# Kernel optimization log

Measured on AMD Instinct MI355X. Metric: run time of the kernel, lower is better.

Reference implementation:

```python
import jax, jax.numpy as jnp
import numpy as np

B, S, DIM, HDIM = 8, 1024, 1024, 128
H = DIM // HDIM  # 8 heads
GN_EPS = 1e-3    # keras GroupNormalization default epsilon


def group_norm(y, gamma, beta, groups, eps=GN_EPS):
    # keras GroupNormalization on [B,S,C]: reshape to [B,S,groups,C//groups],
    # normalize over all axes except batch and group axis -> axes (1,3).
    b, s, c = y.shape
    g = y.reshape(b, s, groups, c // groups)
    mean = g.mean(axis=(1, 3), keepdims=True)
    var = g.var(axis=(1, 3), keepdims=True)
    g = (g - mean) * jax.lax.rsqrt(var + eps)
    return g.reshape(b, s, c) * gamma + beta


def setup_inputs() -> dict:
    key = jax.random.key(0)
    ks = jax.random.split(key, 7)
    x = jax.random.normal(ks[0], (B, S, DIM), dtype=jnp.float32)
    sc_h = 1.0 / np.sqrt(HDIM).astype(np.float32)
    sc_d = 1.0 / np.sqrt(DIM).astype(np.float32)
    Wq = jax.random.normal(ks[1], (H, HDIM, HDIM), dtype=jnp.float32) * sc_h
    Wk = jax.random.normal(ks[2], (H, HDIM, HDIM), dtype=jnp.float32) * sc_h
    Wv = jax.random.normal(ks[3], (H, HDIM, HDIM), dtype=jnp.float32) * sc_h
    Wg = jax.random.normal(ks[4], (DIM, DIM), dtype=jnp.float32) * sc_d
    Wo = jax.random.normal(ks[5], (DIM, DIM), dtype=jnp.float32) * sc_d
    gn_gamma = jnp.ones((DIM,), dtype=jnp.float32)
    gn_beta = jnp.zeros((DIM,), dtype=jnp.float32)
    return {"x": x, "Wq": Wq, "Wk": Wk, "Wv": Wv, "Wg": Wg, "Wo": Wo,
            "gn_gamma": gn_gamma, "gn_beta": gn_beta}


def reference(x, Wq, Wk, Wv, Wg, Wo, gn_gamma, gn_beta):
    b, s, c = x.shape
    h, hd = Wq.shape[0], Wq.shape[1]
    # gating branch: W = ReLU(x @ Wg)
    Wgate = jax.nn.relu(jnp.einsum('bsc,cd->bsd', x, Wg))
    # split channels into heads: [B,S,H,hd]
    xh = x.reshape(b, s, h, hd)
    Q = jnp.einsum('bshd,hde->bhse', xh, Wq)
    K = jnp.einsum('bshd,hde->bhse', xh, Wk)
    V = jnp.einsum('bshd,hde->bhse', xh, Wv)
    # per-head decay mask D[h,i,j] = gamma_h ** (i - j) (full, non-causal as in source)
    idx = jnp.arange(s, dtype=jnp.float32)
    gammas = 1.0 - 2.0 ** (-5.0 - jnp.arange(h, dtype=jnp.float32))  # [H]
    decay = gammas[:, None, None] ** (idx[None, :, None] - idx[None, None, :])  # [H,S,S]
    scores = jnp.einsum('bhsd,bhtd->bhst', Q, K) * decay[None]
    ret = jnp.einsum('bhst,bhtd->bhsd', scores, V)       # [B,H,S,hd]
    y = ret.transpose(0, 2, 1, 3).reshape(b, s, c)        # concat heads
    Y = group_norm(y, gn_gamma, gn_beta, groups=hd)       # groups = hdim (keras arg)
    return jnp.einsum('bsc,cd->bsd', Wgate * Y, Wo)
```

## Files before the change

### kernel.cpp

```cpp
#include <hip/hip_runtime.h>

#define BB 8
#define SS 1024
#define DD 1024
#define HH 8
#define HD 128
#define GN_EPS 1e-3f

typedef __attribute__((ext_vector_type(8))) short bf16x8;
typedef __attribute__((ext_vector_type(4))) float f32x4;

__device__ __forceinline__ short f2bf(float f) {
    unsigned u = __float_as_uint(f);
    return (short)((u + 0x7fffu + ((u >> 16) & 1u)) >> 16);
}
__device__ __forceinline__ float bf2f(short s) {
    return __uint_as_float(((unsigned)(unsigned short)s) << 16);
}

__device__ __forceinline__ void gload16(const void* g, void* l) {
    __builtin_amdgcn_global_load_lds((const __attribute__((address_space(1))) void*)g,
                                     (__attribute__((address_space(3))) void*)l, 16, 0, 0);
}

__device__ __forceinline__ void stage_tile(const short* __restrict__ G, size_t ld, int k0,
                                           short* lds, int wid, int lane) {
#pragma unroll
    for (int i = 0; i < 2; i++) {
        const int seg = wid * 2 + i;
        const int row = seg * 8 + (lane >> 3);
        const int chunk = (lane & 7) ^ (lane >> 3);
        gload16(G + (size_t)row * ld + k0 + chunk * 8, lds + seg * 512);
    }
}

__device__ __forceinline__ void gemm_tile_g(
    const short* __restrict__ A, size_t ldA,
    const short* __restrict__ B, size_t ldB,
    int K, short* As, short* Bs, f32x4 acc[4][2])
{
    const int tid = threadIdx.x, lane = tid & 63, wid = tid >> 6;
    const int wr = (wid >> 2) * 64, wc = (wid & 3) * 32;
    const int fr = lane & 15, fc = lane >> 4;
    const int rsw = fr & 7;
#pragma unroll
    for (int i = 0; i < 4; i++)
#pragma unroll
        for (int j = 0; j < 2; j++) acc[i][j] = (f32x4){0.f, 0.f, 0.f, 0.f};

    const int nt = K >> 6;
    stage_tile(A, ldA, 0, As, wid, lane);
    stage_tile(B, ldB, 0, Bs, wid, lane);
    if (nt > 1) {
        stage_tile(A, ldA, 64, As + 8192, wid, lane);
        stage_tile(B, ldB, 64, Bs + 8192, wid, lane);
    }
    for (int t = 0; t < nt; t++) {
        if (t + 1 < nt) asm volatile("s_waitcnt vmcnt(4)" ::: "memory");
        else            asm volatile("s_waitcnt vmcnt(0)" ::: "memory");
        __builtin_amdgcn_s_barrier();
        __builtin_amdgcn_sched_barrier(0);
        const int cur = t & 1;
        const short* as = As + (cur << 13);
        const short* bs = Bs + (cur << 13);
#pragma unroll
        for (int half = 0; half < 2; half++) {
            const int slot = ((half * 4 + fc) ^ rsw) << 3;
            bf16x8 af[4], bfv[2];
#pragma unroll
            for (int i = 0; i < 4; i++) af[i] = *(const bf16x8*)&as[(wr + i * 16 + fr) * 64 + slot];
#pragma unroll
            for (int j = 0; j < 2; j++) bfv[j] = *(const bf16x8*)&bs[(wc + j * 16 + fr) * 64 + slot];
#pragma unroll
            for (int i = 0; i < 4; i++)
#pragma unroll
                for (int j = 0; j < 2; j++)
                    acc[i][j] = __builtin_amdgcn_mfma_f32_16x16x32_bf16(af[i], bfv[j], acc[i][j], 0, 0, 0);
        }
        __builtin_amdgcn_sched_barrier(0);
        asm volatile("s_waitcnt lgkmcnt(0)" ::: "memory");
        __builtin_amdgcn_s_barrier();
        if (t + 2 < nt) {
            stage_tile(A, ldA, (t + 2) << 6, As + (cur << 13), wid, lane);
            stage_tile(B, ldB, (t + 2) << 6, Bs + (cur << 13), wid, lane);
        }
    }
}

__global__ __launch_bounds__(256) void prep(
    const float* __restrict__ x,
    const float* __restrict__ Wq, const float* __restrict__ Wk, const float* __restrict__ Wv,
    const float* __restrict__ Wg, const float* __restrict__ Wo,
    short* __restrict__ xb, short* __restrict__ WgT, short* __restrict__ WoT,
    short* __restrict__ Wt, float* __restrict__ sQ, float* __restrict__ sK,
    float* __restrict__ Sp)
{
    __shared__ float t[32][33];
    int bid = blockIdx.x;
    const int tid = threadIdx.x;
    if (bid < 4096) {
        const size_t i = ((size_t)bid * 256 + tid) * 8;
        float4 a = *(const float4*)&x[i];
        float4 b = *(const float4*)&x[i + 4];
        bf16x8 v;
        v[0] = f2bf(a.x); v[1] = f2bf(a.y); v[2] = f2bf(a.z); v[3] = f2bf(a.w);
        v[4] = f2bf(b.x); v[5] = f2bf(b.y); v[6] = f2bf(b.z); v[7] = f2bf(b.w);
        *(bf16x8*)&xb[i] = v;
        return;
    }
    bid -= 4096;
    if (bid < 2048) {
        const float* __restrict__ S = (bid < 1024) ? Wg : Wo;
        short* __restrict__ D = (bid < 1024) ? WgT : WoT;
        const int tb = bid & 1023;
        const int bx = (tb & 31) * 32, by = (tb >> 5) * 32;
        const int xx = tid & 31, y0 = tid >> 5;
#pragma unroll
        for (int r = 0; r < 32; r += 8) t[y0 + r][xx] = S[(size_t)(by + y0 + r) * 1024 + bx + xx];
        __syncthreads();
#pragma unroll
        for (int r = 0; r < 32; r += 8) D[(size_t)(bx + y0 + r) * 1024 + by + xx] = f2bf(t[xx][y0 + r]);
        return;
    }
    bid -= 2048;
    if (bid < 384) {
        const int ht = bid >> 4, tb = bid & 15;
        const int typ = ht >> 3, h = ht & 7;
        const float* __restrict__ W = (typ == 0 ? Wq : (typ == 1 ? Wk : Wv)) + (size_t)h * HD * HD;
        short* __restrict__ D = Wt + (size_t)ht * HD * HD;
        const int bx = (tb & 3) * 32, by = (tb >> 2) * 32;
        const int xx = tid & 31, y0 = tid >> 5;
#pragma unroll
        for (int r = 0; r < 32; r += 8) t[y0 + r][xx] = W[(by + y0 + r) * HD + bx + xx];
        __syncthreads();
#pragma unroll
        for (int r = 0; r < 32; r += 8) D[(bx + y0 + r) * HD + by + xx] = f2bf(t[xx][y0 + r]);
        return;
    }
    bid -= 384;
    if (bid < 32) {
        const int h = bid >> 2;
        const int s = (bid & 3) * 256 + tid;
        const double gamma = 1.0 - exp2((double)(-5 - h));
        const double lg = log2(gamma);
        sQ[h * SS + s] = (float)exp2(lg * (double)s);
        sK[h * SS + s] = (float)exp2(-lg * (double)s);
        return;
    }
    *(float4*)&Sp[tid * 8] = (float4){0.f, 0.f, 0.f, 0.f};
    *(float4*)&Sp[tid * 8 + 4] = (float4){0.f, 0.f, 0.f, 0.f};
}

__global__ __launch_bounds__(512) void g_qkvgate(
    const short* __restrict__ xb, const short* __restrict__ Wt, const short* __restrict__ WgT,
    const float* __restrict__ sQ, const float* __restrict__ sK,
    short* __restrict__ Qb, short* __restrict__ Ktb, short* __restrict__ Vtb,
    short* __restrict__ gateb)
{
    __shared__ short As[2 * 8192], Bs[2 * 8192];
    f32x4 acc[4][2];
    const int orig = blockIdx.x;
    const int cx = orig & 7, p = orig >> 3;
    const int tid = threadIdx.x, lane = tid & 63, wid = tid >> 6;
    const int wr = (wid >> 2) * 64, wc = (wid & 3) * 32;
    const int r0 = (lane >> 4) * 4, c = lane & 15;

    if (p < 64) {
        const int w2 = cx * 64 + p;
        const int m0 = (w2 >> 3) * 128, n0 = (w2 & 7) * 128;
        gemm_tile_g(xb + (size_t)m0 * DD, DD, WgT + (size_t)n0 * DD, DD, DD, As, Bs, acc);
#pragma unroll
        for (int i = 0; i < 4; i++)
#pragma unroll
            for (int j = 0; j < 2; j++)
#pragma unroll
                for (int r = 0; r < 4; r++)
                    gateb[(size_t)(m0 + wr + i * 16 + r0 + r) * DD + n0 + wc + j * 16 + c] =
                        f2bf(fmaxf(acc[i][j][r], 0.f));
        return;
    }
    const int w = cx * 192 + (p - 64);
    const int ht = w >> 6, mt = w & 63;
    const int m0 = mt * 128;
    const int typ = ht >> 3, h = ht & 7;
    gemm_tile_g(xb + (size_t)m0 * DD + h * HD, DD,
                Wt + (size_t)ht * HD * HD, HD, HD, As, Bs, acc);
    const int b = m0 >> 10, s0 = m0 & (SS - 1);
    const int bh = (b << 3) + h;
    if (typ == 0) {
#pragma unroll
        for (int i = 0; i < 4; i++)
#pragma unroll
            for (int j = 0; j < 2; j++)
#pragma unroll
                for (int r = 0; r < 4; r++) {
                    const int s = s0 + wr + i * 16 + r0 + r;
                    Qb[((size_t)bh * SS + s) * HD + wc + j * 16 + c] =
                        f2bf(acc[i][j][r] * sQ[h * SS + s]);
                }
    } else if (typ == 1) {
        short* __restrict__ Ob = Ktb + (size_t)bh * HD * SS;
#pragma unroll
        for (int i = 0; i < 4; i++)
#pragma unroll
            for (int j = 0; j < 2; j++) {
                const int tb = s0 + wr + i * 16 + r0;
                const int d = wc + j * 16 + c;
                short4 o;
                o.x = f2bf(acc[i][j][0] * sK[h * SS + tb + 0]);
                o.y = f2bf(acc[i][j][1] * sK[h * SS + tb + 1]);
                o.z = f2bf(acc[i][j][2] * sK[h * SS + tb + 2]);
                o.w = f2bf(acc[i][j][3] * sK[h * SS + tb + 3]);
                *(short4*)&Ob[(size_t)d * SS + tb] = o;
            }
    } else {
        short* __restrict__ Ob = Vtb + (size_t)bh * HD * SS;
#pragma unroll
        for (int i = 0; i < 4; i++)
#pragma unroll
            for (int j = 0; j < 2; j++) {
                const int tb = s0 + wr + i * 16 + r0;
                const int e = wc + j * 16 + c;
                short4 o;
                o.x = f2bf(acc[i][j][0]); o.y = f2bf(acc[i][j][1]);
                o.z = f2bf(acc[i][j][2]); o.w = f2bf(acc[i][j][3]);
                *(short4*)&Ob[(size_t)e * SS + tb] = o;
            }
    }
}

__global__ __launch_bounds__(512) void g_kv(
    const short* __restrict__ Vtb, const short* __restrict__ Ktb, float* __restrict__ Mp)
{
    __shared__ short As[2 * 8192], Bs[2 * 8192];
    f32x4 acc[4][2];
    const int orig = blockIdx.x;
    const int w = (orig & 7) * 32 + (orig >> 3);
    const int chunk = w & 3, bh = w >> 2;
    gemm_tile_g(Vtb + (size_t)bh * HD * SS + chunk * 256, SS,
                Ktb + (size_t)bh * HD * SS + chunk * 256, SS, 256, As, Bs, acc);
    const int tid = threadIdx.x, lane = tid & 63, wid = tid >> 6;
    const int wr = (wid >> 2) * 64, wc = (wid & 3) * 32;
    const int r0 = (lane >> 4) * 4, c = lane & 15;
    float* __restrict__ Ob = Mp + (size_t)w * HD * HD;
#pragma unroll
    for (int i = 0; i < 4; i++)
#pragma unroll
        for (int j = 0; j < 2; j++)
#pragma unroll
            for (int r = 0; r < 4; r++)
                Ob[(size_t)(wr + i * 16 + r0 + r) * HD + wc + j * 16 + c] = acc[i][j][r];
}

__global__ __launch_bounds__(256) void g_mredcvt(const float* __restrict__ Mp, short* __restrict__ Mtb) {
    const size_t i = ((size_t)blockIdx.x * 256 + threadIdx.x) * 8;
    const size_t bh = i >> 14, ij = i & 16383;
    const float* p = Mp + (bh * 4) * 16384 + ij;
    float s[8];
#pragma unroll
    for (int q = 0; q < 8; q++) s[q] = 0.f;
#pragma unroll
    for (int cth = 0; cth < 4; cth++) {
        float4 a = *(const float4*)&p[cth * 16384];
        float4 b = *(const float4*)&p[cth * 16384 + 4];
        s[0] += a.x; s[1] += a.y; s[2] += a.z; s[3] += a.w;
        s[4] += b.x; s[5] += b.y; s[6] += b.z; s[7] += b.w;
    }
    bf16x8 v;
#pragma unroll
    for (int q = 0; q < 8; q++) v[q] = f2bf(s[q]);
    *(bf16x8*)&Mtb[i] = v;
}

__global__ __launch_bounds__(512) void g_qm(
    const short* __restrict__ Qb, const short* __restrict__ Mtb,
    short* __restrict__ retc, float* __restrict__ Sp)
{
    __shared__ short As[2 * 8192], Bs[2 * 8192];
    f32x4 acc[4][2];
    const int orig = blockIdx.x;
    const int w = (orig & 7) * 64 + (orig >> 3);
    const int bh = w >> 3, m0 = (w & 7) * 128;
    gemm_tile_g(Qb + ((size_t)bh * SS + m0) * HD, HD,
                Mtb + (size_t)bh * HD * HD, HD, HD, As, Bs, acc);
    const int tid = threadIdx.x, lane = tid & 63, wid = tid >> 6;
    const int wr = (wid >> 2) * 64, wc = (wid & 3) * 32;
    const int r0 = (lane >> 4) * 4, c = lane & 15;
    const int b_ = bh >> 3, h_ = bh & 7;
    short* __restrict__ O = retc + ((size_t)(b_ * SS + m0)) * DD + h_ * HD;
#pragma unroll
    for (int i = 0; i < 4; i++)
#pragma unroll
        for (int j = 0; j < 2; j++)
#pragma unroll
            for (int r = 0; r < 4; r++)
                O[(size_t)(wr + i * 16 + r0 + r) * DD + wc + j * 16 + c] = f2bf(acc[i][j][r]);

    float psm[2], psq[2];
#pragma unroll
    for (int j = 0; j < 2; j++) { psm[j] = 0.f; psq[j] = 0.f; }
#pragma unroll
    for (int i = 0; i < 4; i++)
#pragma unroll
        for (int j = 0; j < 2; j++)
#pragma unroll
            for (int r = 0; r < 4; r++) {
                const float v = acc[i][j][r];
                psm[j] += v; psq[j] += v * v;
            }
    const int masks[5] = {1, 2, 4, 16, 32};
#pragma unroll
    for (int mk = 0; mk < 5; mk++) {
#pragma unroll
        for (int j = 0; j < 2; j++) {
            psm[j] += __shfl_xor(psm[j], masks[mk], 64);
            psq[j] += __shfl_xor(psq[j], masks[mk], 64);
        }
    }
    if ((lane & 7) == 0 && lane < 16) {
        const int hi = lane >> 3;
#pragma unroll
        for (int j = 0; j < 2; j++) {
            const int g = b_ * 128 + h_ * 16 + (wid & 3) * 4 + j * 2 + hi;
            atomicAdd(&Sp[g * 2 + 0], psm[j]);
            atomicAdd(&Sp[g * 2 + 1], psq[j]);
        }
    }
}

__global__ __launch_bounds__(256) void aprep(
    const short* __restrict__ gateb, const short* __restrict__ retc,
    const float* __restrict__ Sp,
    const float* __restrict__ gng, const float* __restrict__ gnb, short* __restrict__ Ab)
{
    const size_t idx = ((size_t)blockIdx.x * 256 + threadIdx.x) * 4;
    const int m = (int)(idx >> 10), cc = (int)(idx & 1023);
    const int b_ = m >> 10, g = b_ * 128 + (cc >> 3);
    const float sm = Sp[g * 2 + 0], sq = Sp[g * 2 + 1];
    const float mu = sm * (1.0f / 8192.0f);
    float var = sq * (1.0f / 8192.0f) - mu * mu;
    if (var < 0.f) var = 0.f;
    const float rs = rsqrtf(var + GN_EPS);
    short4 gv4 = *(const short4*)&gateb[idx];
    short4 rv4 = *(const short4*)&retc[idx];
    float4 gv = *(const float4*)&gng[cc];
    float4 bv = *(const float4*)&gnb[cc];
    short4 o;
    o.x = f2bf(bf2f(gv4.x) * ((bf2f(rv4.x) - mu) * rs * gv.x + bv.x));
    o.y = f2bf(bf2f(gv4.y) * ((bf2f(rv4.y) - mu) * rs * gv.y + bv.y));
    o.z = f2bf(bf2f(gv4.z) * ((bf2f(rv4.z) - mu) * rs * gv.z + bv.z));
    o.w = f2bf(bf2f(gv4.w) * ((bf2f(rv4.w) - mu) * rs * gv.w + bv.w));
    *(short4*)&Ab[idx] = o;
}

__global__ __launch_bounds__(512) void g_final(
    const short* __restrict__ Ab, const short* __restrict__ WoT, float* __restrict__ out)
{
    __shared__ short As[2 * 8192], Bs[2 * 8192];
    f32x4 acc[4][2];
    const int orig = blockIdx.x;
    const int w = (orig & 7) * 64 + (orig >> 3);
    const int m0 = (w >> 3) * 128, n0 = (w & 7) * 128;
    gemm_tile_g(Ab + (size_t)m0 * DD, DD, WoT + (size_t)n0 * DD, DD, DD, As, Bs, acc);
    const int tid = threadIdx.x, lane = tid & 63, wid = tid >> 6;
    const int wr = (wid >> 2) * 64, wc = (wid & 3) * 32;
    const int r0 = (lane >> 4) * 4, c = lane & 15;
#pragma unroll
    for (int i = 0; i < 4; i++)
#pragma unroll
        for (int j = 0; j < 2; j++)
#pragma unroll
            for (int r = 0; r < 4; r++)
                out[(size_t)(m0 + wr + i * 16 + r0 + r) * DD + n0 + wc + j * 16 + c] = acc[i][j][r];
}

extern "C" void kernel_launch(void* const* d_in, const int* in_sizes, int n_in,
                              void* d_out, int out_size, void* d_ws, size_t ws_size,
                              hipStream_t stream)
{
    const float* x   = (const float*)d_in[0];
    const float* Wq  = (const float*)d_in[1];
    const float* Wk  = (const float*)d_in[2];
    const float* Wv  = (const float*)d_in[3];
    const float* Wg  = (const float*)d_in[4];
    const float* Wo  = (const float*)d_in[5];
    const float* gng = (const float*)d_in[6];
    const float* gnb = (const float*)d_in[7];
    float* out = (float*)d_out;

    char* ws = (char*)d_ws;
    size_t off = 0;
    auto alloc = [&](size_t bytes) -> void* {
        void* p = ws + off;
        off += (bytes + 255) & ~(size_t)255;
        return p;
    };
    const size_t NE = (size_t)BB * SS * DD;
    float*  sQ    = (float*)alloc((size_t)HH * SS * sizeof(float));
    float*  sK    = (float*)alloc((size_t)HH * SS * sizeof(float));
    short*  xb    = (short*)alloc(NE * sizeof(short));
    short*  WgT   = (short*)alloc((size_t)DD * DD * sizeof(short));
    short*  WoT   = (short*)alloc((size_t)DD * DD * sizeof(short));
    short*  Wt    = (short*)alloc((size_t)24 * HD * HD * sizeof(short));
    short*  Qb    = (short*)alloc(NE * sizeof(short));
    short*  Ktb   = (short*)alloc(NE * sizeof(short));
    short*  Vtb   = (short*)alloc(NE * sizeof(short));
    short*  retc  = (short*)alloc(NE * sizeof(short));
    short*  gateb = (short*)alloc(NE * sizeof(short));
    short*  Ab    = (short*)alloc(NE * sizeof(short));
    float*  Mp    = (float*)alloc((size_t)256 * HD * HD * sizeof(float));
    short*  Mtb   = (short*)alloc((size_t)64 * HD * HD * sizeof(short));
    float*  Sp    = (float*)alloc((size_t)1024 * 2 * sizeof(float));

    prep<<<dim3(6561), 256, 0, stream>>>(x, Wq, Wk, Wv, Wg, Wo, xb, WgT, WoT, Wt, sQ, sK, Sp);
    g_qkvgate<<<dim3(2048), 512, 0, stream>>>(xb, Wt, WgT, sQ, sK, Qb, Ktb, Vtb, gateb);
    g_kv<<<dim3(256), 512, 0, stream>>>(Vtb, Ktb, Mp);
    g_mredcvt<<<dim3(512), 256, 0, stream>>>(Mp, Mtb);
    g_qm<<<dim3(512), 512, 0, stream>>>(Qb, Mtb, retc, Sp);
    aprep<<<dim3(8192), 256, 0, stream>>>(gateb, retc, Sp, gng, gnb, Ab);
    g_final<<<dim3(512), 512, 0, stream>>>(Ab, WoT, out);
}
```

Baseline: 117.5 us.

## Compute Q, K and V projections in one block reusing the staged x tile

```diff
diff --git a/kernel.cpp b/kernel.cpp
--- a/kernel.cpp
+++ b/kernel.cpp
@@ -179,53 +179,99 @@
                         f2bf(fmaxf(acc[i][j][r], 0.f));
         return;
     }
-    const int w = cx * 192 + (p - 64);
-    const int ht = w >> 6, mt = w & 63;
+    const int w = cx * 64 + (p - 64);
+    const int mt = w >> 3, h = w & 7;
     const int m0 = mt * 128;
-    const int typ = ht >> 3, h = ht & 7;
-    gemm_tile_g(xb + (size_t)m0 * DD + h * HD, DD,
-                Wt + (size_t)ht * HD * HD, HD, HD, As, Bs, acc);
     const int b = m0 >> 10, s0 = m0 & (SS - 1);
     const int bh = (b << 3) + h;
-    if (typ == 0) {
-#pragma unroll
-        for (int i = 0; i < 4; i++)
-#pragma unroll
-            for (int j = 0; j < 2; j++)
-#pragma unroll
-                for (int r = 0; r < 4; r++) {
-                    const int s = s0 + wr + i * 16 + r0 + r;
-                    Qb[((size_t)bh * SS + s) * HD + wc + j * 16 + c] =
-                        f2bf(acc[i][j][r] * sQ[h * SS + s]);
-                }
-    } else if (typ == 1) {
-        short* __restrict__ Ob = Ktb + (size_t)bh * HD * SS;
-#pragma unroll
-        for (int i = 0; i < 4; i++)
-#pragma unroll
-            for (int j = 0; j < 2; j++) {
-                const int tb = s0 + wr + i * 16 + r0;
-                const int d = wc + j * 16 + c;
-                short4 o;
-                o.x = f2bf(acc[i][j][0] * sK[h * SS + tb + 0]);
-                o.y = f2bf(acc[i][j][1] * sK[h * SS + tb + 1]);
-                o.z = f2bf(acc[i][j][2] * sK[h * SS + tb + 2]);
-                o.w = f2bf(acc[i][j][3] * sK[h * SS + tb + 3]);
-                *(short4*)&Ob[(size_t)d * SS + tb] = o;
+    const short* __restrict__ A = xb + (size_t)m0 * DD + h * HD;
+
+    const int fr = lane & 15, fc = lane >> 4;
+    const int rsw = fr & 7;
+
+    stage_tile(A, DD, 0,  As,        wid, lane);
+    stage_tile(A, DD, 64, As + 8192, wid, lane);
+    stage_tile(Wt + (size_t)h * HD * HD, HD, 0, Bs, wid, lane);
+    __syncthreads();
+
+#pragma unroll
+    for (int i = 0; i < 4; i++)
+#pragma unroll
+        for (int j = 0; j < 2; j++) acc[i][j] = (f32x4){0.f, 0.f, 0.f, 0.f};
+
+    int sb = 0;
+    for (int st = 0; st < 6; st++) {
+        if (st + 1 < 6) {
+            const int typn = (st + 1) >> 1, ktn = (st + 1) & 1;
+            stage_tile(Wt + (size_t)(typn * 8 + h) * HD * HD, HD, ktn * 64,
+                       Bs + ((sb ^ 1) << 13), wid, lane);
+        }
+        const int kt = st & 1;
+        const short* as = As + (kt << 13);
+        const short* bs = Bs + (sb << 13);
+#pragma unroll
+        for (int half = 0; half < 2; half++) {
+            const int slot = ((half * 4 + fc) ^ rsw) << 3;
+            bf16x8 af[4], bfv[2];
+#pragma unroll
+            for (int i = 0; i < 4; i++) af[i] = *(const bf16x8*)&as[(wr + i * 16 + fr) * 64 + slot];
+#pragma unroll
+            for (int j = 0; j < 2; j++) bfv[j] = *(const bf16x8*)&bs[(wc + j * 16 + fr) * 64 + slot];
+#pragma unroll
+            for (int i = 0; i < 4; i++)
+#pragma unroll
+                for (int j = 0; j < 2; j++)
+                    acc[i][j] = __builtin_amdgcn_mfma_f32_16x16x32_bf16(af[i], bfv[j], acc[i][j], 0, 0, 0);
+        }
+        __syncthreads();
+        sb ^= 1;
+        if (kt == 1) {
+            const int typ = st >> 1;
+            if (typ == 0) {
+#pragma unroll
+                for (int i = 0; i < 4; i++)
+#pragma unroll
+                    for (int j = 0; j < 2; j++)
+#pragma unroll
+                        for (int r = 0; r < 4; r++) {
+                            const int s = s0 + wr + i * 16 + r0 + r;
+                            Qb[((size_t)bh * SS + s) * HD + wc + j * 16 + c] =
+                                f2bf(acc[i][j][r] * sQ[h * SS + s]);
+                        }
+            } else if (typ == 1) {
+                short* __restrict__ Ob = Ktb + (size_t)bh * HD * SS;
+#pragma unroll
+                for (int i = 0; i < 4; i++)
+#pragma unroll
+                    for (int j = 0; j < 2; j++) {
+                        const int tb = s0 + wr + i * 16 + r0;
+                        const int d = wc + j * 16 + c;
+                        short4 o;
+                        o.x = f2bf(acc[i][j][0] * sK[h * SS + tb + 0]);
+                        o.y = f2bf(acc[i][j][1] * sK[h * SS + tb + 1]);
+                        o.z = f2bf(acc[i][j][2] * sK[h * SS + tb + 2]);
+                        o.w = f2bf(acc[i][j][3] * sK[h * SS + tb + 3]);
+                        *(short4*)&Ob[(size_t)d * SS + tb] = o;
+                    }
+            } else {
+                short* __restrict__ Ob = Vtb + (size_t)bh * HD * SS;
+#pragma unroll
+                for (int i = 0; i < 4; i++)
+#pragma unroll
+                    for (int j = 0; j < 2; j++) {
+                        const int tb = s0 + wr + i * 16 + r0;
+                        const int e = wc + j * 16 + c;
+                        short4 o;
+                        o.x = f2bf(acc[i][j][0]); o.y = f2bf(acc[i][j][1]);
+                        o.z = f2bf(acc[i][j][2]); o.w = f2bf(acc[i][j][3]);
+                        *(short4*)&Ob[(size_t)e * SS + tb] = o;
+                    }
             }
-    } else {
-        short* __restrict__ Ob = Vtb + (size_t)bh * HD * SS;
-#pragma unroll
-        for (int i = 0; i < 4; i++)
-#pragma unroll
-            for (int j = 0; j < 2; j++) {
-                const int tb = s0 + wr + i * 16 + r0;
-                const int e = wc + j * 16 + c;
-                short4 o;
-                o.x = f2bf(acc[i][j][0]); o.y = f2bf(acc[i][j][1]);
-                o.z = f2bf(acc[i][j][2]); o.w = f2bf(acc[i][j][3]);
-                *(short4*)&Ob[(size_t)e * SS + tb] = o;
-            }
+#pragma unroll
+            for (int i = 0; i < 4; i++)
+#pragma unroll
+                for (int j = 0; j < 2; j++) acc[i][j] = (f32x4){0.f, 0.f, 0.f, 0.f};
+        }
     }
 }
 
@@ -413,7 +459,7 @@
     float*  Sp    = (float*)alloc((size_t)1024 * 2 * sizeof(float));
 
     prep<<<dim3(6561), 256, 0, stream>>>(x, Wq, Wk, Wv, Wg, Wo, xb, WgT, WoT, Wt, sQ, sK, Sp);
-    g_qkvgate<<<dim3(2048), 512, 0, stream>>>(xb, Wt, WgT, sQ, sK, Qb, Ktb, Vtb, gateb);
+    g_qkvgate<<<dim3(1024), 512, 0, stream>>>(xb, Wt, WgT, sQ, sK, Qb, Ktb, Vtb, gateb);
     g_kv<<<dim3(256), 512, 0, stream>>>(Vtb, Ktb, Mp);
     g_mredcvt<<<dim3(512), 256, 0, stream>>>(Mp, Mtb);
     g_qm<<<dim3(512), 512, 0, stream>>>(Qb, Mtb, retc, Sp);
```

Result: faster. 113.6 us (-3.3%).
